# Kernel tuning notes

Measured on AMD Instinct MI355X. Metric: run time of the kernel, lower is better.

## Reference

```python
import jax, jax.numpy as jnp
from jax import lax
import numpy as np

B, CIN, H, W = 1, 3, 96, 96
Q = 65536
C = 64
CU = C * 9              # feat_unfold channels
IN_DIM = CU + 2 + 2     # q_feat + rel_coord + rel_cell
HID = 256
OUT = 3
EPS_SHIFT = 1e-6


def setup_inputs():
    key = jax.random.key(0)
    ks = jax.random.split(key, 16)
    inp = jax.random.normal(ks[0], (B, CIN, H, W), jnp.float32)
    coord = jax.random.uniform(ks[1], (B, Q, 2), jnp.float32, -1.0, 1.0)
    cell = jnp.full((B, Q, 2), 2.0 / 256.0, jnp.float32)  # cell size of a 256x256 output grid
    enc_w = jax.random.normal(ks[2], (C, CIN, 3, 3), jnp.float32) * 0.1
    enc_b = jnp.zeros((C,), jnp.float32)
    dims = [IN_DIM, HID, HID, HID, HID, OUT]
    out = {"inp": inp, "coord": coord, "cell": cell, "enc_w": enc_w, "enc_b": enc_b}
    for i in range(5):
        out[f"w{i}"] = jax.random.normal(ks[3 + i], (dims[i], dims[i + 1]), jnp.float32) * (1.0 / np.sqrt(dims[i]))
        out[f"b{i}"] = jnp.zeros((dims[i + 1],), jnp.float32)
    return out


def _unfold3x3(feat):
    # F.unfold(feat, 3, padding=1).reshape(b, c*9, h, w): channel order c-major, kernel row-major
    b, c, h, w = feat.shape
    p = jnp.pad(feat, ((0, 0), (0, 0), (1, 1), (1, 1)))
    pats = jnp.stack([p[:, :, ki:ki + h, kj:kj + w] for ki in range(3) for kj in range(3)], axis=2)
    return pats.reshape(b, c * 9, h, w)


def _nearest_idx(c, n):
    # torch grid_sample nearest, align_corners=False: unnormalize then round-half-even (nearbyint)
    ix = (c + 1.0) * n / 2.0 - 0.5
    return jnp.clip(jnp.round(ix), 0, n - 1).astype(jnp.int32)


def _gather(fmap, iy, ix):
    # fmap [B,C,H,W], iy/ix [B,Q] -> [B,Q,C]
    return jax.vmap(lambda f, y, x: f[:, y, x].T)(fmap, iy, ix)


def _mlp(x, ws, bs):
    for wgt, b in zip(ws[:-1], bs[:-1]):
        x = jax.nn.relu(x @ wgt + b)
    return x @ ws[-1] + bs[-1]


def reference(inp, coord, cell, enc_w, enc_b, w0, b0, w1, b1, w2, b2, w3, b3, w4, b4):
    ws = [w0, w1, w2, w3, w4]
    bs = [b0, b1, b2, b3, b4]
    # encoder: 3x3 conv, SAME padding
    feat = lax.conv_general_dilated(inp, enc_w, (1, 1), 'SAME') + enc_b[None, :, None, None]
    feat = _unfold3x3(feat)                     # [B, C*9, H, W]
    h, w = feat.shape[2], feat.shape[3]
    rx, ry = 1.0 / h, 1.0 / w                   # 2/r/2
    # make_coord pixel centers
    fcy = -1.0 + (2.0 * jnp.arange(h, dtype=jnp.float32) + 1.0) / h   # [H]
    fcx = -1.0 + (2.0 * jnp.arange(w, dtype=jnp.float32) + 1.0) / w   # [W]
    bnd = 1.0 - 1e-6
    rel_cell = cell * jnp.array([h, w], dtype=cell.dtype)             # [B,Q,2]

    preds, areas = [], []
    for vx in (-1.0, 1.0):
        for vy in (-1.0, 1.0):
            c0 = jnp.clip(coord[..., 0] + vx * rx + EPS_SHIFT, -bnd, bnd)
            c1 = jnp.clip(coord[..., 1] + vy * ry + EPS_SHIFT, -bnd, bnd)
            iy = _nearest_idx(c0, h)            # coord[...,0] indexes dim H
            ix = _nearest_idx(c1, w)
            q_feat = _gather(feat, iy, ix)      # [B,Q,CU]
            rel0 = (coord[..., 0] - fcy[iy]) * h
            rel1 = (coord[..., 1] - fcx[ix]) * w
            mlp_in = jnp.concatenate([q_feat, rel0[..., None], rel1[..., None], rel_cell], axis=-1)
            pred = _mlp(mlp_in.reshape(-1, IN_DIM), ws, bs).reshape(coord.shape[0], coord.shape[1], OUT)
            preds.append(pred)
            areas.append(jnp.abs(rel0 * rel1) + 1e-9)

    tot_area = areas[0] + areas[1] + areas[2] + areas[3]
    # local-ensemble diagonal swap
    areas = [areas[3], areas[2], areas[1], areas[0]]
    ret = 0.0
    for pred, area in zip(preds, areas):
        ret = ret + pred * (area / tot_area)[..., None]
    return ret
```

## Files before the change

### kernel.cpp

```cpp
#include <hip/hip_runtime.h>
#include <math.h>

#define NPOS 9216

using half8 = __attribute__((ext_vector_type(8))) _Float16;
using f32x4 = __attribute__((ext_vector_type(4))) float;

__global__ __launch_bounds__(256) void conv_kernel(const float* __restrict__ inp,
                                                   const float* __restrict__ enc_w,
                                                   const float* __restrict__ enc_b,
                                                   float* __restrict__ feat)
{
    int idx = blockIdx.x * 256 + threadIdx.x;
    if (idx >= 64 * NPOS) return;
    int c   = idx / NPOS;
    int rem = idx - c * NPOS;
    int y   = rem / 96;
    int x   = rem - y * 96;
    float acc = enc_b[c];
    #pragma unroll
    for (int cin = 0; cin < 3; ++cin) {
        #pragma unroll
        for (int ky = 0; ky < 3; ++ky) {
            int yy = y + ky - 1;
            if (yy < 0 || yy >= 96) continue;
            #pragma unroll
            for (int kx = 0; kx < 3; ++kx) {
                int xx = x + kx - 1;
                if (xx < 0 || xx >= 96) continue;
                acc = fmaf(inp[cin * NPOS + yy * 96 + xx],
                           enc_w[c * 27 + cin * 9 + ky * 3 + kx], acc);
            }
        }
    }
    feat[idx] = acc;
}

__global__ __launch_bounds__(256) void a0_kernel(const float* __restrict__ feat,
                                                 const float* __restrict__ w0,
                                                 const float* __restrict__ b0,
                                                 float* __restrict__ A0)
{
    __shared__ float win[64][3][10];
    const int t   = threadIdx.x;
    const int blk = blockIdx.x;
    const int y   = blk / 12;
    const int x0  = (blk - y * 12) * 8;

    for (int i = t; i < 64 * 30; i += 256) {
        int c   = i / 30;
        int rem = i - c * 30;
        int dy  = rem / 10;
        int dx  = rem - dy * 10;
        int gy  = y + dy - 1;
        int gx  = x0 + dx - 1;
        float v = 0.0f;
        if (gy >= 0 && gy < 96 && gx >= 0 && gx < 96)
            v = feat[c * NPOS + gy * 96 + gx];
        win[c][dy][dx] = v;
    }
    __syncthreads();

    float acc[8];
    float bv = b0[t];
    #pragma unroll
    for (int p = 0; p < 8; ++p) acc[p] = bv;

    for (int c = 0; c < 64; ++c) {
        #pragma unroll
        for (int t9 = 0; t9 < 9; ++t9) {
            int ki = t9 / 3;
            int kj = t9 - ki * 3;
            float wv = w0[(c * 9 + t9) * 256 + t];
            #pragma unroll
            for (int p = 0; p < 8; ++p)
                acc[p] = fmaf(win[c][ki][kj + p], wv, acc[p]);
        }
    }
    #pragma unroll
    for (int p = 0; p < 8; ++p)
        A0[(y * 96 + x0 + p) * 256 + t] = acc[p];
}

__global__ __launch_bounds__(256) void pack_w(const float* __restrict__ w1,
                                              const float* __restrict__ w2,
                                              const float* __restrict__ w3,
                                              const float* __restrict__ w4,
                                              _Float16* __restrict__ wf)
{
    int idx = blockIdx.x * 256 + threadIdx.x;
    if (idx < 3 * 65536) {
        int l = idx >> 16;
        int r = idx & 65535;
        int j    = r & 7;
        int lane = (r >> 3) & 63;
        int ntB  = (r >> 9) & 15;
        int ks   = r >> 13;
        int n = ntB * 16 + (lane & 15);
        int k = ks * 32 + (lane >> 4) * 8 + j;
        const float* W = (l == 0) ? w1 : (l == 1) ? w2 : w3;
        wf[idx] = (_Float16)W[k * 256 + n];
    } else if (idx < 3 * 65536 + 4096) {
        int r = idx - 3 * 65536;
        int j    = r & 7;
        int lane = (r >> 3) & 63;
        int ks   = r >> 9;
        int n = lane & 15;
        int k = ks * 32 + (lane >> 4) * 8 + j;
        wf[idx] = (n < 3) ? (_Float16)w4[k * 3 + n] : (_Float16)0.0f;
    }
}

__device__ __forceinline__ void hidden_mfma(_Float16 (*h)[264],
                                            const _Float16* __restrict__ W,
                                            const float* __restrict__ bias,
                                            int wm, int wn, int lane)
{
    const int l15 = lane & 15;
    const int l4  = lane >> 4;
    f32x4 acc[4][4];
    #pragma unroll
    for (int mt = 0; mt < 4; ++mt)
        #pragma unroll
        for (int nt = 0; nt < 4; ++nt)
            acc[mt][nt] = (f32x4){0.f, 0.f, 0.f, 0.f};

    #pragma unroll
    for (int ks = 0; ks < 8; ++ks) {
        half8 a[4], b[4];
        #pragma unroll
        for (int mt = 0; mt < 4; ++mt)
            a[mt] = *(const half8*)&h[wm * 64 + mt * 16 + l15][ks * 32 + l4 * 8];
        #pragma unroll
        for (int nt = 0; nt < 4; ++nt)
            b[nt] = *(const half8*)&W[((ks * 16 + wn * 4 + nt) * 64 + lane) * 8];
        #pragma unroll
        for (int mt = 0; mt < 4; ++mt)
            #pragma unroll
            for (int nt = 0; nt < 4; ++nt)
                acc[mt][nt] = __builtin_amdgcn_mfma_f32_16x16x32_f16(a[mt], b[nt], acc[mt][nt], 0, 0, 0);
    }
    __syncthreads();
    #pragma unroll
    for (int nt = 0; nt < 4; ++nt) {
        int col = wn * 64 + nt * 16 + l15;
        float bv = bias[col];
        #pragma unroll
        for (int mt = 0; mt < 4; ++mt) {
            int rowb = wm * 64 + mt * 16 + l4 * 4;
            #pragma unroll
            for (int i = 0; i < 4; ++i)
                h[rowb + i][col] = (_Float16)fmaxf(acc[mt][nt][i] + bv, 0.0f);
        }
    }
    __syncthreads();
}

__global__ __launch_bounds__(512, 4) void fused_kernel(
    const float* __restrict__ A0, const float* __restrict__ coord,
    const float* __restrict__ cell, const float* __restrict__ w0,
    const float* __restrict__ b1, const float* __restrict__ b2,
    const float* __restrict__ b3, const float* __restrict__ b4,
    const _Float16* __restrict__ wf,
    float* __restrict__ out)
{
    __shared__ _Float16 h[128][264];
    __shared__ float pred[128][4];
    __shared__ float s_rel0[128], s_rel1[128], s_rc0[128], s_rc1[128], s_area[128];
    __shared__ int   s_pos[128];

    const int t   = threadIdx.x;
    const int blk = blockIdx.x;

    if (t < 128) {
        int r = blk * 128 + t;
        int q = r >> 2;
        int j = r & 3;
        float vx = (j & 2) ? 1.0f : -1.0f;
        float vy = (j & 1) ? 1.0f : -1.0f;
        float c0 = coord[q * 2 + 0];
        float c1 = coord[q * 2 + 1];
        const float rr  = 1.0f / 96.0f;
        const float bnd = 1.0f - 1e-6f;
        float sc0 = fminf(fmaxf(fmaf(vx, rr, c0) + 1e-6f, -bnd), bnd);
        float sc1 = fminf(fmaxf(fmaf(vy, rr, c1) + 1e-6f, -bnd), bnd);
        float fy = (sc0 + 1.0f) * 48.0f - 0.5f;
        float fx = (sc1 + 1.0f) * 48.0f - 0.5f;
        int iy = (int)rintf(fy); iy = iy < 0 ? 0 : (iy > 95 ? 95 : iy);
        int ix = (int)rintf(fx); ix = ix < 0 ? 0 : (ix > 95 ? 95 : ix);
        float fcy = -1.0f + (2.0f * (float)iy + 1.0f) / 96.0f;
        float fcx = -1.0f + (2.0f * (float)ix + 1.0f) / 96.0f;
        float rel0 = (c0 - fcy) * 96.0f;
        float rel1 = (c1 - fcx) * 96.0f;
        s_pos[t]  = iy * 96 + ix;
        s_rel0[t] = rel0;
        s_rel1[t] = rel1;
        s_rc0[t]  = cell[q * 2 + 0] * 96.0f;
        s_rc1[t]  = cell[q * 2 + 1] * 96.0f;
        s_area[t] = fabsf(rel0 * rel1) + 1e-9f;
    }
    __syncthreads();

    {
        int col = t & 255;
        int m0  = (t >> 8) * 64;
        float wa = w0[576 * 256 + col];
        float wb = w0[577 * 256 + col];
        float wc = w0[578 * 256 + col];
        float wd = w0[579 * 256 + col];
        #pragma unroll 4
        for (int mm = 0; mm < 64; ++mm) {
            int m = m0 + mm;
            float v = A0[s_pos[m] * 256 + col];
            v = fmaf(s_rel0[m], wa, v);
            v = fmaf(s_rel1[m], wb, v);
            v = fmaf(s_rc0[m], wc, v);
            v = fmaf(s_rc1[m], wd, v);
            h[m][col] = (_Float16)fmaxf(v, 0.0f);
        }
    }
    __syncthreads();

    const int wave = t >> 6;
    const int lane = t & 63;
    const int wm = wave >> 2;
    const int wn = wave & 3;

    hidden_mfma(h, wf,             b1, wm, wn, lane);
    hidden_mfma(h, wf + 65536,     b2, wm, wn, lane);
    hidden_mfma(h, wf + 2 * 65536, b3, wm, wn, lane);

    {
        const int l15 = lane & 15;
        const int l4  = lane >> 4;
        const _Float16* W4 = wf + 3 * 65536;
        f32x4 acc = (f32x4){0.f, 0.f, 0.f, 0.f};
        #pragma unroll
        for (int ks = 0; ks < 8; ++ks) {
            half8 a = *(const half8*)&h[wave * 16 + l15][ks * 32 + l4 * 8];
            half8 b = *(const half8*)&W4[(ks * 64 + lane) * 8];
            acc = __builtin_amdgcn_mfma_f32_16x16x32_f16(a, b, acc, 0, 0, 0);
        }
        if (l15 < 3) {
            float bv = b4[l15];
            #pragma unroll
            for (int i = 0; i < 4; ++i)
                pred[wave * 16 + l4 * 4 + i][l15] = acc[i] + bv;
        }
    }
    __syncthreads();

    if (t < 96) {
        int ql = t / 3;
        int o  = t - ql * 3;
        int mb = ql * 4;
        float a0 = s_area[mb + 0];
        float a1 = s_area[mb + 1];
        float a2 = s_area[mb + 2];
        float a3 = s_area[mb + 3];
        float tot = a0 + a1 + a2 + a3;
        float rv = pred[mb + 0][o] * a3 + pred[mb + 1][o] * a2 +
                   pred[mb + 2][o] * a1 + pred[mb + 3][o] * a0;
        out[(blk * 32 + ql) * 3 + o] = rv / tot;
    }
}

extern "C" void kernel_launch(void* const* d_in, const int* in_sizes, int n_in,
                              void* d_out, int out_size, void* d_ws, size_t ws_size,
                              hipStream_t stream)
{
    (void)in_sizes; (void)n_in; (void)out_size; (void)ws_size;
    const float* inp   = (const float*)d_in[0];
    const float* coord = (const float*)d_in[1];
    const float* cell  = (const float*)d_in[2];
    const float* enc_w = (const float*)d_in[3];
    const float* enc_b = (const float*)d_in[4];
    const float* w0 = (const float*)d_in[5];
    const float* b0 = (const float*)d_in[6];
    const float* w1 = (const float*)d_in[7];
    const float* b1 = (const float*)d_in[8];
    const float* w2 = (const float*)d_in[9];
    const float* b2 = (const float*)d_in[10];
    const float* w3 = (const float*)d_in[11];
    const float* b3 = (const float*)d_in[12];
    const float* w4 = (const float*)d_in[13];
    const float* b4 = (const float*)d_in[14];
    float* outp = (float*)d_out;

    float*    feat = (float*)d_ws;
    float*    A0   = feat + 64 * NPOS;
    _Float16* wf   = (_Float16*)(A0 + NPOS * 256);

    conv_kernel<<<dim3((64 * NPOS + 255) / 256), dim3(256), 0, stream>>>(inp, enc_w, enc_b, feat);
    a0_kernel<<<dim3(96 * 12), dim3(256), 0, stream>>>(feat, w0, b0, A0);
    pack_w<<<dim3((3 * 65536 + 4096 + 255) / 256), dim3(256), 0, stream>>>(w1, w2, w3, w4, wf);
    fused_kernel<<<dim3(2048), dim3(512), 0, stream>>>(A0, coord, cell, w0,
                                                       b1, b2, b3, b4, wf, outp);
}
```

Measured before the change: 279.6 us.

## Use MFMA for first layer, 32x32 MFMA tiles, fp16 A0, merged setup kernel

Replaces the scalar FP32 first-layer precompute with an MFMA kernel over a padded, channel-last fp16 feature map and a repacked fp16 w0. A0 is stored in fp16, which halves the gather traffic in the fused kernel. The hidden layers switch from 16x16x32 to 32x32x16 MFMA with a new weight packing, and conv plus all packing is merged into one setup launch. The cost is extra fp16 rounding of A0 and the features, plus accumulator register pressure in the new kernels.

```diff
diff --git a/kernel.cpp b/kernel.cpp
--- a/kernel.cpp
+++ b/kernel.cpp
@@ -3,165 +3,182 @@
 
 #define NPOS 9216
 
-using half8 = __attribute__((ext_vector_type(8))) _Float16;
-using f32x4 = __attribute__((ext_vector_type(4))) float;
-
-__global__ __launch_bounds__(256) void conv_kernel(const float* __restrict__ inp,
-                                                   const float* __restrict__ enc_w,
-                                                   const float* __restrict__ enc_b,
-                                                   float* __restrict__ feat)
-{
-    int idx = blockIdx.x * 256 + threadIdx.x;
-    if (idx >= 64 * NPOS) return;
-    int c   = idx / NPOS;
-    int rem = idx - c * NPOS;
-    int y   = rem / 96;
-    int x   = rem - y * 96;
-    float acc = enc_b[c];
-    #pragma unroll
-    for (int cin = 0; cin < 3; ++cin) {
-        #pragma unroll
-        for (int ky = 0; ky < 3; ++ky) {
-            int yy = y + ky - 1;
-            if (yy < 0 || yy >= 96) continue;
+using half8  = __attribute__((ext_vector_type(8))) _Float16;
+using f32x4  = __attribute__((ext_vector_type(4))) float;
+using f32x16 = __attribute__((ext_vector_type(16))) float;
+
+#define OFF_FEATT 0u
+#define OFF_A0    1229312u
+#define OFF_WF32  5947904u
+#define OFF_WF4   6341120u
+#define OFF_WB    6349312u
+
+#define NB_FEAT 2401
+#define NB_PA   768
+#define NB_PW4  16
+#define NB_PB   576
+
+__global__ __launch_bounds__(256) void setup_kernel(
+    const float* __restrict__ inp, const float* __restrict__ enc_w,
+    const float* __restrict__ enc_b, const float* __restrict__ w0,
+    const float* __restrict__ w1, const float* __restrict__ w2,
+    const float* __restrict__ w3, const float* __restrict__ w4,
+    _Float16* __restrict__ featT, _Float16* __restrict__ wf32,
+    _Float16* __restrict__ wf4, _Float16* __restrict__ wB)
+{
+    int blk = blockIdx.x;
+    const int t = threadIdx.x;
+
+    if (blk < NB_FEAT) {
+        int pp = blk * 4 + (t >> 6);
+        int c  = t & 63;
+        int py = pp / 98, px = pp - py * 98;
+        float acc = 0.0f;
+        if (py >= 1 && py <= 96 && px >= 1 && px <= 96) {
+            int y = py - 1, x = px - 1;
+            acc = enc_b[c];
             #pragma unroll
-            for (int kx = 0; kx < 3; ++kx) {
-                int xx = x + kx - 1;
-                if (xx < 0 || xx >= 96) continue;
-                acc = fmaf(inp[cin * NPOS + yy * 96 + xx],
-                           enc_w[c * 27 + cin * 9 + ky * 3 + kx], acc);
+            for (int cin = 0; cin < 3; ++cin) {
+                #pragma unroll
+                for (int ky = 0; ky < 3; ++ky) {
+                    int yy = y + ky - 1;
+                    if (yy < 0 || yy >= 96) continue;
+                    #pragma unroll
+                    for (int kx = 0; kx < 3; ++kx) {
+                        int xx = x + kx - 1;
+                        if (xx < 0 || xx >= 96) continue;
+                        acc = fmaf(inp[cin * NPOS + yy * 96 + xx],
+                                   enc_w[c * 27 + cin * 9 + ky * 3 + kx], acc);
+                    }
+                }
             }
         }
-    }
-    feat[idx] = acc;
-}
-
-__global__ __launch_bounds__(256) void a0_kernel(const float* __restrict__ feat,
-                                                 const float* __restrict__ w0,
-                                                 const float* __restrict__ b0,
-                                                 float* __restrict__ A0)
-{
-    __shared__ float win[64][3][10];
-    const int t   = threadIdx.x;
-    const int blk = blockIdx.x;
-    const int y   = blk / 12;
-    const int x0  = (blk - y * 12) * 8;
-
-    for (int i = t; i < 64 * 30; i += 256) {
-        int c   = i / 30;
-        int rem = i - c * 30;
-        int dy  = rem / 10;
-        int dx  = rem - dy * 10;
-        int gy  = y + dy - 1;
-        int gx  = x0 + dx - 1;
-        float v = 0.0f;
-        if (gy >= 0 && gy < 96 && gx >= 0 && gx < 96)
-            v = feat[c * NPOS + gy * 96 + gx];
-        win[c][dy][dx] = v;
-    }
-    __syncthreads();
-
-    float acc[8];
-    float bv = b0[t];
-    #pragma unroll
-    for (int p = 0; p < 8; ++p) acc[p] = bv;
-
-    for (int c = 0; c < 64; ++c) {
-        #pragma unroll
-        for (int t9 = 0; t9 < 9; ++t9) {
-            int ki = t9 / 3;
-            int kj = t9 - ki * 3;
-            float wv = w0[(c * 9 + t9) * 256 + t];
-            #pragma unroll
-            for (int p = 0; p < 8; ++p)
-                acc[p] = fmaf(win[c][ki][kj + p], wv, acc[p]);
-        }
-    }
-    #pragma unroll
-    for (int p = 0; p < 8; ++p)
-        A0[(y * 96 + x0 + p) * 256 + t] = acc[p];
-}
-
-__global__ __launch_bounds__(256) void pack_w(const float* __restrict__ w1,
-                                              const float* __restrict__ w2,
-                                              const float* __restrict__ w3,
-                                              const float* __restrict__ w4,
-                                              _Float16* __restrict__ wf)
-{
-    int idx = blockIdx.x * 256 + threadIdx.x;
-    if (idx < 3 * 65536) {
+        featT[pp * 64 + c] = (_Float16)acc;
+        return;
+    }
+    blk -= NB_FEAT;
+    if (blk < NB_PA) {
+        int idx = blk * 256 + t;
         int l = idx >> 16;
         int r = idx & 65535;
         int j    = r & 7;
         int lane = (r >> 3) & 63;
-        int ntB  = (r >> 9) & 15;
-        int ks   = r >> 13;
+        int nt32 = (r >> 9) & 7;
+        int ks   = r >> 12;
+        int n = nt32 * 32 + (lane & 31);
+        int k = ks * 16 + ((lane >> 5) << 3) + j;
+        const float* W = (l == 0) ? w1 : (l == 1) ? w2 : w3;
+        wf32[idx] = (_Float16)W[k * 256 + n];
+        return;
+    }
+    blk -= NB_PA;
+    if (blk < NB_PW4) {
+        int idx = blk * 256 + t;
+        int j    = idx & 7;
+        int lane = (idx >> 3) & 63;
+        int ks   = idx >> 9;
+        int n = lane & 15;
+        int k = ks * 32 + ((lane >> 4) << 3) + j;
+        wf4[idx] = (n < 3) ? (_Float16)w4[k * 3 + n] : (_Float16)0.0f;
+        return;
+    }
+    blk -= NB_PW4;
+    {
+        int idx = blk * 256 + t;
+        int j    = idx & 7;
+        int lane = (idx >> 3) & 63;
+        int ntB  = (idx >> 9) & 15;
+        int ks   = (idx >> 13) & 1;
+        int t9   = idx >> 14;
+        int c = ks * 32 + ((lane >> 4) << 3) + j;
         int n = ntB * 16 + (lane & 15);
-        int k = ks * 32 + (lane >> 4) * 8 + j;
-        const float* W = (l == 0) ? w1 : (l == 1) ? w2 : w3;
-        wf[idx] = (_Float16)W[k * 256 + n];
-    } else if (idx < 3 * 65536 + 4096) {
-        int r = idx - 3 * 65536;
-        int j    = r & 7;
-        int lane = (r >> 3) & 63;
-        int ks   = r >> 9;
-        int n = lane & 15;
-        int k = ks * 32 + (lane >> 4) * 8 + j;
-        wf[idx] = (n < 3) ? (_Float16)w4[k * 3 + n] : (_Float16)0.0f;
-    }
-}
-
-__device__ __forceinline__ void hidden_mfma(_Float16 (*h)[264],
-                                            const _Float16* __restrict__ W,
-                                            const float* __restrict__ bias,
-                                            int wm, int wn, int lane)
-{
-    const int l15 = lane & 15;
-    const int l4  = lane >> 4;
-    f32x4 acc[4][4];
-    #pragma unroll
-    for (int mt = 0; mt < 4; ++mt)
+        wB[idx] = (_Float16)w0[(c * 9 + t9) * 256 + n];
+    }
+}
+
+__global__ __launch_bounds__(256) void a0_mfma(const _Float16* __restrict__ featT,
+                                               const _Float16* __restrict__ wB,
+                                               const float* __restrict__ b0,
+                                               _Float16* __restrict__ A0)
+{
+    const int lane = threadIdx.x & 63;
+    const int tile = blockIdx.x * 4 + (threadIdx.x >> 6);
+    const int l15  = lane & 15;
+    const int l4   = lane >> 4;
+    int r = tile * 16 + l15;
+    int y = r / 96, x = r - y * 96;
+
+    f32x4 acc[16];
+    #pragma unroll
+    for (int nt = 0; nt < 16; ++nt) acc[nt] = (f32x4){0.f, 0.f, 0.f, 0.f};
+
+    #pragma unroll
+    for (int t9 = 0; t9 < 9; ++t9) {
+        int ki = t9 / 3, kj = t9 - ki * 3;
+        const _Float16* ap = featT + ((y + ki) * 98 + (x + kj)) * 64 + l4 * 8;
         #pragma unroll
-        for (int nt = 0; nt < 4; ++nt)
-            acc[mt][nt] = (f32x4){0.f, 0.f, 0.f, 0.f};
-
-    #pragma unroll
-    for (int ks = 0; ks < 8; ++ks) {
-        half8 a[4], b[4];
+        for (int ks = 0; ks < 2; ++ks) {
+            half8 a = *(const half8*)(ap + ks * 32);
+            const _Float16* bp = wB + ((t9 * 2 + ks) * 16 * 64 + lane) * 8;
+            #pragma unroll
+            for (int nt = 0; nt < 16; ++nt) {
+                half8 b = *(const half8*)(bp + nt * 512);
+                acc[nt] = __builtin_amdgcn_mfma_f32_16x16x32_f16(a, b, acc[nt], 0, 0, 0);
+            }
+        }
+    }
+    int rb = tile * 16 + l4 * 4;
+    #pragma unroll
+    for (int nt = 0; nt < 16; ++nt) {
+        float bb = b0[nt * 16 + l15];
         #pragma unroll
-        for (int mt = 0; mt < 4; ++mt)
-            a[mt] = *(const half8*)&h[wm * 64 + mt * 16 + l15][ks * 32 + l4 * 8];
-        #pragma unroll
-        for (int nt = 0; nt < 4; ++nt)
-            b[nt] = *(const half8*)&W[((ks * 16 + wn * 4 + nt) * 64 + lane) * 8];
-        #pragma unroll
-        for (int mt = 0; mt < 4; ++mt)
-            #pragma unroll
-            for (int nt = 0; nt < 4; ++nt)
-                acc[mt][nt] = __builtin_amdgcn_mfma_f32_16x16x32_f16(a[mt], b[nt], acc[mt][nt], 0, 0, 0);
-    }
-    __syncthreads();
-    #pragma unroll
-    for (int nt = 0; nt < 4; ++nt) {
-        int col = wn * 64 + nt * 16 + l15;
-        float bv = bias[col];
-        #pragma unroll
-        for (int mt = 0; mt < 4; ++mt) {
-            int rowb = wm * 64 + mt * 16 + l4 * 4;
-            #pragma unroll
-            for (int i = 0; i < 4; ++i)
-                h[rowb + i][col] = (_Float16)fmaxf(acc[mt][nt][i] + bv, 0.0f);
-        }
+        for (int i = 0; i < 4; ++i)
+            A0[(rb + i) * 256 + nt * 16 + l15] = (_Float16)(acc[nt][i] + bb);
+    }
+}
+
+__device__ __forceinline__ void hidden32(_Float16 (*h)[264],
+                                         const _Float16* __restrict__ W,
+                                         const float* __restrict__ bias,
+                                         int wm, int wn, int lane)
+{
+    const int l31 = lane & 31;
+    const int l5  = lane >> 5;
+    f32x16 a00 = {}, a01 = {}, a10 = {}, a11 = {};
+    #pragma unroll
+    for (int ks = 0; ks < 16; ++ks) {
+        half8 Av0 = *(const half8*)&h[wm * 64 + l31][ks * 16 + l5 * 8];
+        half8 Av1 = *(const half8*)&h[wm * 64 + 32 + l31][ks * 16 + l5 * 8];
+        const _Float16* bp = W + (ks * 8 + wn * 2) * 512 + lane * 8;
+        half8 Bv0 = *(const half8*)bp;
+        half8 Bv1 = *(const half8*)(bp + 512);
+        a00 = __builtin_amdgcn_mfma_f32_32x32x16_f16(Av0, Bv0, a00, 0, 0, 0);
+        a01 = __builtin_amdgcn_mfma_f32_32x32x16_f16(Av0, Bv1, a01, 0, 0, 0);
+        a10 = __builtin_amdgcn_mfma_f32_32x32x16_f16(Av1, Bv0, a10, 0, 0, 0);
+        a11 = __builtin_amdgcn_mfma_f32_32x32x16_f16(Av1, Bv1, a11, 0, 0, 0);
+    }
+    __syncthreads();
+    float bv0 = bias[wn * 64 + l31];
+    float bv1 = bias[wn * 64 + 32 + l31];
+    #pragma unroll
+    for (int reg = 0; reg < 16; ++reg) {
+        int rr = (reg & 3) + ((reg >> 2) << 3) + (l5 << 2);
+        int r0 = wm * 64 + rr;
+        int c0 = wn * 64 + l31;
+        h[r0][c0]           = (_Float16)fmaxf(a00[reg] + bv0, 0.0f);
+        h[r0][c0 + 32]      = (_Float16)fmaxf(a01[reg] + bv1, 0.0f);
+        h[r0 + 32][c0]      = (_Float16)fmaxf(a10[reg] + bv0, 0.0f);
+        h[r0 + 32][c0 + 32] = (_Float16)fmaxf(a11[reg] + bv1, 0.0f);
     }
     __syncthreads();
 }
 
 __global__ __launch_bounds__(512, 4) void fused_kernel(
-    const float* __restrict__ A0, const float* __restrict__ coord,
+    const _Float16* __restrict__ A0, const float* __restrict__ coord,
     const float* __restrict__ cell, const float* __restrict__ w0,
     const float* __restrict__ b1, const float* __restrict__ b2,
     const float* __restrict__ b3, const float* __restrict__ b4,
-    const _Float16* __restrict__ wf,
+    const _Float16* __restrict__ wf32, const _Float16* __restrict__ wf4,
     float* __restrict__ out)
 {
     __shared__ _Float16 h[128][264];
@@ -211,7 +228,7 @@
         #pragma unroll 4
         for (int mm = 0; mm < 64; ++mm) {
             int m = m0 + mm;
-            float v = A0[s_pos[m] * 256 + col];
+            float v = (float)A0[s_pos[m] * 256 + col];
             v = fmaf(s_rel0[m], wa, v);
             v = fmaf(s_rel1[m], wb, v);
             v = fmaf(s_rc0[m], wc, v);
@@ -226,19 +243,18 @@
     const int wm = wave >> 2;
     const int wn = wave & 3;
 
-    hidden_mfma(h, wf,             b1, wm, wn, lane);
-    hidden_mfma(h, wf + 65536,     b2, wm, wn, lane);
-    hidden_mfma(h, wf + 2 * 65536, b3, wm, wn, lane);
+    hidden32(h, wf32,             b1, wm, wn, lane);
+    hidden32(h, wf32 + 65536,     b2, wm, wn, lane);
+    hidden32(h, wf32 + 2 * 65536, b3, wm, wn, lane);
 
     {
         const int l15 = lane & 15;
         const int l4  = lane >> 4;
-        const _Float16* W4 = wf + 3 * 65536;
         f32x4 acc = (f32x4){0.f, 0.f, 0.f, 0.f};
         #pragma unroll
         for (int ks = 0; ks < 8; ++ks) {
             half8 a = *(const half8*)&h[wave * 16 + l15][ks * 32 + l4 * 8];
-            half8 b = *(const half8*)&W4[(ks * 64 + lane) * 8];
+            half8 b = *(const half8*)&wf4[(ks * 64 + lane) * 8];
             acc = __builtin_amdgcn_mfma_f32_16x16x32_f16(a, b, acc, 0, 0, 0);
         }
         if (l15 < 3) {
@@ -287,13 +303,16 @@
     const float* b4 = (const float*)d_in[14];
     float* outp = (float*)d_out;
 
-    float*    feat = (float*)d_ws;
-    float*    A0   = feat + 64 * NPOS;
-    _Float16* wf   = (_Float16*)(A0 + NPOS * 256);
-
-    conv_kernel<<<dim3((64 * NPOS + 255) / 256), dim3(256), 0, stream>>>(inp, enc_w, enc_b, feat);
-    a0_kernel<<<dim3(96 * 12), dim3(256), 0, stream>>>(feat, w0, b0, A0);
-    pack_w<<<dim3((3 * 65536 + 4096 + 255) / 256), dim3(256), 0, stream>>>(w1, w2, w3, w4, wf);
+    char* ws = (char*)d_ws;
+    _Float16* featT = (_Float16*)(ws + OFF_FEATT);
+    _Float16* A0    = (_Float16*)(ws + OFF_A0);
+    _Float16* wf32  = (_Float16*)(ws + OFF_WF32);
+    _Float16* wf4   = (_Float16*)(ws + OFF_WF4);
+    _Float16* wB    = (_Float16*)(ws + OFF_WB);
+
+    setup_kernel<<<dim3(NB_FEAT + NB_PA + NB_PW4 + NB_PB), dim3(256), 0, stream>>>(
+        inp, enc_w, enc_b, w0, w1, w2, w3, w4, featT, wf32, wf4, wB);
+    a0_mfma<<<dim3(144), dim3(256), 0, stream>>>(featT, wB, b0, A0);
     fused_kernel<<<dim3(2048), dim3(512), 0, stream>>>(A0, coord, cell, w0,
-                                                       b1, b2, b3, b4, wf, outp);
-}
+                                                       b1, b2, b3, b4, wf32, wf4, outp);
+}
```

Result: slower. 304.7 us (+8.9%).
